# Kernel optimization log

Hardware: AMD Instinct MI355X
Metric: run time of the kernel (lower is better)

Reference implementation:

```python
import jax, jax.numpy as jnp
import numpy as np
from jax import lax

EPS = 1e-06
S = 0.025
ALPHA = 0.98
DELTA = 2.0
R = 0.5


def setup_inputs() -> dict:
    key = jax.random.key(0)
    # magnitude spectrogram: [batch, freq, time], nonnegative
    x = jax.random.uniform(key, (32, 256, 4096), dtype=jnp.float32)
    return {"x": x}


def reference(x):
    # x: [B, F, T]; EMA smoother runs over the time axis (last dim).
    # m_0 = s*x_0 ; m_t = (1-s)*m_{t-1} + s*x_t  (init carry 0 reproduces m_0 = s*x_0)
    xt = jnp.moveaxis(x, 2, 0)  # [T, B, F]

    def step(m, frame):
        m = (1.0 - S) * m + S * frame
        return m, m

    _, M = lax.scan(step, jnp.zeros_like(xt[0]), xt)  # [T, B, F]
    M = jnp.moveaxis(M, 0, 2)  # [B, F, T]
    # power-law compression fused elementwise
    return (x / (M + EPS) ** ALPHA + DELTA) ** R - DELTA ** R
```

## Files before the change

### kernel.cpp

```cpp
#include <hip/hip_runtime.h>


constexpr int T_LEN  = 4096;
constexpr int NTHR   = 1024;
constexpr int PER    = 4;

constexpr float EPSF = 1e-6f;
constexpr float SF   = 0.025f;
constexpr float A1F  = 0.975f;

constexpr double dA1   = 0.975;
constexpr double dA2   = dA1 * dA1;
constexpr double dA4   = dA2 * dA2;
constexpr double dA8   = dA4 * dA4;
constexpr double dA16  = dA8 * dA8;
constexpr double dA32  = dA16 * dA16;
constexpr double dA64  = dA32 * dA32;
constexpr double dA128 = dA64 * dA64;
constexpr double dA256 = dA128 * dA128;

__global__ __launch_bounds__(NTHR) void pcen_scan_kernel(
    const float* __restrict__ x, float* __restrict__ out)
{
    const int row  = blockIdx.x;
    const long long base = (long long)row * T_LEN;
    const int tid  = threadIdx.x;
    const int lane = tid & 63;
    const int wave = tid >> 6;

    const float4* __restrict__ px   = (const float4*)(x + base);
    float4* __restrict__       pout = (float4*)(out + base);

    float4 v = px[tid];
    float xv[PER] = { v.x, v.y, v.z, v.w };

    float m = 0.0f;
#pragma unroll
    for (int k = 0; k < PER; ++k) m = fmaf(A1F, m, SF * xv[k]);
    float Sv = m;

    const float c1  = (float)dA4;
    const float c2  = (float)dA8;
    const float c4  = (float)dA16;
    const float c8  = (float)dA32;
    const float c16 = (float)dA64;
    const float c32 = (float)dA128;
    const float c64 = (float)dA256;
    float t;
    t = __shfl_up(Sv, 1,  64); if (lane >= 1)  Sv = fmaf(c1,  t, Sv);
    t = __shfl_up(Sv, 2,  64); if (lane >= 2)  Sv = fmaf(c2,  t, Sv);
    t = __shfl_up(Sv, 4,  64); if (lane >= 4)  Sv = fmaf(c4,  t, Sv);
    t = __shfl_up(Sv, 8,  64); if (lane >= 8)  Sv = fmaf(c8,  t, Sv);
    t = __shfl_up(Sv, 16, 64); if (lane >= 16) Sv = fmaf(c16, t, Sv);
    t = __shfl_up(Sv, 32, 64); if (lane >= 32) Sv = fmaf(c32, t, Sv);

    __shared__ float Wt[NTHR / 64];
    if (lane == 63) Wt[wave] = Sv;
    __syncthreads();
    float cw = 0.0f;
    for (int u = 0; u < wave; ++u) cw = fmaf(c64, cw, Wt[u]);

    {
        int e = lane + 1;
        float f = 1.0f;
        if (e & 1)  f *= c1;
        if (e & 2)  f *= c2;
        if (e & 4)  f *= c4;
        if (e & 8)  f *= c8;
        if (e & 16) f *= c16;
        if (e & 32) f *= c32;
        if (e & 64) f *= c64;
        Sv = fmaf(f, cw, Sv);
    }
    float carry = __shfl_up(Sv, 1, 64);
    if (lane == 0) carry = cw;

    const float SQRT_D = 1.41421356237309515f;
    float r[PER];
    m = carry;
#pragma unroll
    for (int k = 0; k < PER; ++k) {
        m = fmaf(A1F, m, SF * xv[k]);
        float p = __builtin_amdgcn_exp2f(-0.98f * __builtin_amdgcn_logf(m + EPSF));
        r[k] = __fsqrt_rn(fmaf(xv[k], p, 2.0f)) - SQRT_D;
    }

    pout[tid] = make_float4(r[0], r[1], r[2], r[3]);
}

extern "C" void kernel_launch(void* const* d_in, const int* in_sizes, int n_in,
                              void* d_out, int out_size, void* d_ws, size_t ws_size,
                              hipStream_t stream) {
    const float* x = (const float*)d_in[0];
    float* out = (float*)d_out;
    const int rows = in_sizes[0] / T_LEN;
    pcen_scan_kernel<<<dim3(rows), dim3(NTHR), 0, stream>>>(x, out);
}
```

Baseline: 225.0 us.

## Process each row with a single wave using chunked scan and prefetch

Each row was handled by a 1024-thread block doing one scan plus a cross-wave LDS pass and barrier. Now one 64-lane wave owns a whole row and walks it in four chunks of 1024 elements. Each lane serially scans 16 elements, then a wave-level shuffle scan combines the lanes, and a carry passes between chunks. The next chunk is loaded into registers while the current one is computed. This removes __syncthreads and LDS traffic, but each lane now does longer serial dependency chains and holds more registers, and the row count gives only 8192/4 blocks of small size.

New measurement: 244.7 us. +8.8%, slower.

```diff
diff --git a/kernel.cpp b/kernel.cpp
--- a/kernel.cpp
+++ b/kernel.cpp
@@ -2,90 +2,132 @@
 
 
 constexpr int T_LEN  = 4096;
-constexpr int NTHR   = 1024;
-constexpr int PER    = 4;
+constexpr int LANES  = 64;
+constexpr int QUADS  = 4;
+constexpr int PER_LANE = QUADS * 4;
+constexpr int CHUNK  = LANES * PER_LANE;
+constexpr int CHUNK_F4 = CHUNK / 4;
+constexpr int NCHUNK = T_LEN / CHUNK;
+constexpr int WAVES_PER_BLK = 4;
+constexpr int NTHR   = LANES * WAVES_PER_BLK;
 
 constexpr float EPSF = 1e-6f;
 constexpr float SF   = 0.025f;
 constexpr float A1F  = 0.975f;
 
-constexpr double dA1   = 0.975;
-constexpr double dA2   = dA1 * dA1;
-constexpr double dA4   = dA2 * dA2;
-constexpr double dA8   = dA4 * dA4;
-constexpr double dA16  = dA8 * dA8;
-constexpr double dA32  = dA16 * dA16;
-constexpr double dA64  = dA32 * dA32;
-constexpr double dA128 = dA64 * dA64;
-constexpr double dA256 = dA128 * dA128;
+constexpr double dA1    = 0.975;
+constexpr double dA2    = dA1 * dA1;
+constexpr double dA4    = dA2 * dA2;
+constexpr double dA8    = dA4 * dA4;
+constexpr double dA16   = dA8 * dA8;
+constexpr double dA32   = dA16 * dA16;
+constexpr double dA64   = dA32 * dA32;
+constexpr double dA128  = dA64 * dA64;
+constexpr double dA256  = dA128 * dA128;
+constexpr double dA512  = dA256 * dA256;
+constexpr double dA1024 = dA512 * dA512;
 
-__global__ __launch_bounds__(NTHR) void pcen_scan_kernel(
-    const float* __restrict__ x, float* __restrict__ out)
+__global__ __launch_bounds__(NTHR, 6) void pcen_wave_kernel(
+    const float* __restrict__ x, float* __restrict__ out, int rows)
 {
-    const int row  = blockIdx.x;
+    const int lane = threadIdx.x & 63;
+    const int wave = threadIdx.x >> 6;
+    const int row  = blockIdx.x * WAVES_PER_BLK + wave;
+    if (row >= rows) return;
+
     const long long base = (long long)row * T_LEN;
-    const int tid  = threadIdx.x;
-    const int lane = tid & 63;
-    const int wave = tid >> 6;
-
     const float4* __restrict__ px   = (const float4*)(x + base);
     float4* __restrict__       pout = (float4*)(out + base);
 
-    float4 v = px[tid];
-    float xv[PER] = { v.x, v.y, v.z, v.w };
+    const float cA16  = (float)dA16;
+    const float cA32  = (float)dA32;
+    const float cA64  = (float)dA64;
+    const float cA128 = (float)dA128;
+    const float cA256 = (float)dA256;
+    const float cA512 = (float)dA512;
+    const float cA1024 = (float)dA1024;
 
-    float m = 0.0f;
-#pragma unroll
-    for (int k = 0; k < PER; ++k) m = fmaf(A1F, m, SF * xv[k]);
-    float Sv = m;
-
-    const float c1  = (float)dA4;
-    const float c2  = (float)dA8;
-    const float c4  = (float)dA16;
-    const float c8  = (float)dA32;
-    const float c16 = (float)dA64;
-    const float c32 = (float)dA128;
-    const float c64 = (float)dA256;
-    float t;
-    t = __shfl_up(Sv, 1,  64); if (lane >= 1)  Sv = fmaf(c1,  t, Sv);
-    t = __shfl_up(Sv, 2,  64); if (lane >= 2)  Sv = fmaf(c2,  t, Sv);
-    t = __shfl_up(Sv, 4,  64); if (lane >= 4)  Sv = fmaf(c4,  t, Sv);
-    t = __shfl_up(Sv, 8,  64); if (lane >= 8)  Sv = fmaf(c8,  t, Sv);
-    t = __shfl_up(Sv, 16, 64); if (lane >= 16) Sv = fmaf(c16, t, Sv);
-    t = __shfl_up(Sv, 32, 64); if (lane >= 32) Sv = fmaf(c32, t, Sv);
-
-    __shared__ float Wt[NTHR / 64];
-    if (lane == 63) Wt[wave] = Sv;
-    __syncthreads();
-    float cw = 0.0f;
-    for (int u = 0; u < wave; ++u) cw = fmaf(c64, cw, Wt[u]);
-
-    {
-        int e = lane + 1;
-        float f = 1.0f;
-        if (e & 1)  f *= c1;
-        if (e & 2)  f *= c2;
-        if (e & 4)  f *= c4;
-        if (e & 8)  f *= c8;
-        if (e & 16) f *= c16;
-        if (e & 32) f *= c32;
-        if (e & 64) f *= c64;
-        Sv = fmaf(f, cw, Sv);
-    }
-    float carry = __shfl_up(Sv, 1, 64);
-    if (lane == 0) carry = cw;
+    float flane = 1.0f;
+    if (lane & 1)  flane *= cA16;
+    if (lane & 2)  flane *= cA32;
+    if (lane & 4)  flane *= cA64;
+    if (lane & 8)  flane *= cA128;
+    if (lane & 16) flane *= cA256;
+    if (lane & 32) flane *= cA512;
 
     const float SQRT_D = 1.41421356237309515f;
-    float r[PER];
-    m = carry;
+
+    float4 buf[QUADS];
+    {
+        const float4* p = px + lane * QUADS;
 #pragma unroll
-    for (int k = 0; k < PER; ++k) {
-        m = fmaf(A1F, m, SF * xv[k]);
-        float p = __builtin_amdgcn_exp2f(-0.98f * __builtin_amdgcn_logf(m + EPSF));
-        r[k] = __fsqrt_rn(fmaf(xv[k], p, 2.0f)) - SQRT_D;
+        for (int j = 0; j < QUADS; ++j) buf[j] = p[j];
     }
 
-    pout[tid] = make_float4(r[0], r[1], r[2], r[3]);
+    float carry = 0.0f;
+
+#pragma unroll
+    for (int c = 0; c < NCHUNK; ++c) {
+        float4 nxt[QUADS];
+        if (c < NCHUNK - 1) {
+            const float4* p = px + (c + 1) * CHUNK_F4 + lane * QUADS;
+#pragma unroll
+            for (int j = 0; j < QUADS; ++j) nxt[j] = p[j];
+        }
+
+        float m = 0.0f;
+#pragma unroll
+        for (int j = 0; j < QUADS; ++j) {
+            m = fmaf(A1F, m, SF * buf[j].x);
+            m = fmaf(A1F, m, SF * buf[j].y);
+            m = fmaf(A1F, m, SF * buf[j].z);
+            m = fmaf(A1F, m, SF * buf[j].w);
+        }
+        float Sv = m;
+
+        float t;
+        t = __shfl_up(Sv, 1,  64); if (lane >= 1)  Sv = fmaf(cA16,  t, Sv);
+        t = __shfl_up(Sv, 2,  64); if (lane >= 2)  Sv = fmaf(cA32,  t, Sv);
+        t = __shfl_up(Sv, 4,  64); if (lane >= 4)  Sv = fmaf(cA64,  t, Sv);
+        t = __shfl_up(Sv, 8,  64); if (lane >= 8)  Sv = fmaf(cA128, t, Sv);
+        t = __shfl_up(Sv, 16, 64); if (lane >= 16) Sv = fmaf(cA256, t, Sv);
+        t = __shfl_up(Sv, 32, 64); if (lane >= 32) Sv = fmaf(cA512, t, Sv);
+
+        float excl = __shfl_up(Sv, 1, 64);
+        if (lane == 0) excl = 0.0f;
+
+        m = fmaf(flane, carry, excl);
+
+        float last = __shfl(Sv, 63, 64);
+        carry = fmaf(cA1024, carry, last);
+
+        float4* q = pout + c * CHUNK_F4 + lane * QUADS;
+#pragma unroll
+        for (int j = 0; j < QUADS; ++j) {
+            float4 v = buf[j];
+            float4 o;
+            m = fmaf(A1F, m, SF * v.x);
+            o.x = __builtin_amdgcn_sqrtf(
+                      fmaf(v.x, __builtin_amdgcn_exp2f(
+                          -0.98f * __builtin_amdgcn_logf(m + EPSF)), 2.0f)) - SQRT_D;
+            m = fmaf(A1F, m, SF * v.y);
+            o.y = __builtin_amdgcn_sqrtf(
+                      fmaf(v.y, __builtin_amdgcn_exp2f(
+                          -0.98f * __builtin_amdgcn_logf(m + EPSF)), 2.0f)) - SQRT_D;
+            m = fmaf(A1F, m, SF * v.z);
+            o.z = __builtin_amdgcn_sqrtf(
+                      fmaf(v.z, __builtin_amdgcn_exp2f(
+                          -0.98f * __builtin_amdgcn_logf(m + EPSF)), 2.0f)) - SQRT_D;
+            m = fmaf(A1F, m, SF * v.w);
+            o.w = __builtin_amdgcn_sqrtf(
+                      fmaf(v.w, __builtin_amdgcn_exp2f(
+                          -0.98f * __builtin_amdgcn_logf(m + EPSF)), 2.0f)) - SQRT_D;
+            q[j] = o;
+        }
+
+#pragma unroll
+        for (int j = 0; j < QUADS; ++j) buf[j] = nxt[j];
+    }
 }
 
 extern "C" void kernel_launch(void* const* d_in, const int* in_sizes, int n_in,
@@ -94,5 +136,6 @@
     const float* x = (const float*)d_in[0];
     float* out = (float*)d_out;
     const int rows = in_sizes[0] / T_LEN;
-    pcen_scan_kernel<<<dim3(rows), dim3(NTHR), 0, stream>>>(x, out);
+    const int blocks = (rows + WAVES_PER_BLK - 1) / WAVES_PER_BLK;
+    pcen_wave_kernel<<<dim3(blocks), dim3(NTHR), 0, stream>>>(x, out, rows);
 }
```
